# Optimization experiments

Hardware: AMD Instinct MI355X
Metric: run time of the kernel (lower is better)

Reference implementation:

```python
import jax, jax.numpy as jnp
import numpy as np

B, P, Q, O, H = 2048, 32, 65, 16, 32

def setup_inputs() -> dict:
    key = jax.random.key(0)
    ks = jax.random.split(key, 13)
    s1 = 1.0           # fan_in = 1 for Linear(1,H)
    sH = 1.0 / np.sqrt(H)
    return {
        "x": jax.random.normal(ks[0], (B, P), dtype=jnp.float32),
        # psi_{p,q}: 1 -> H -> H -> 1 MLPs, stacked over (P, Q)
        "psi_w1": jax.random.normal(ks[1], (P, Q, H), dtype=jnp.float32) * s1,
        "psi_b1": jax.random.normal(ks[2], (P, Q, H), dtype=jnp.float32) * s1,
        "psi_w2": jax.random.normal(ks[3], (P, Q, H, H), dtype=jnp.float32) * sH,
        "psi_b2": jax.random.normal(ks[4], (P, Q, H), dtype=jnp.float32) * sH,
        "psi_w3": jax.random.normal(ks[5], (P, Q, H), dtype=jnp.float32) * sH,
        "psi_b3": jax.random.normal(ks[6], (P, Q), dtype=jnp.float32) * sH,
        # phi_{q,i}: 1 -> H -> H -> 1 MLPs, stacked over (Q, O)
        "phi_w1": jax.random.normal(ks[7], (Q, O, H), dtype=jnp.float32) * s1,
        "phi_b1": jax.random.normal(ks[8], (Q, O, H), dtype=jnp.float32) * s1,
        "phi_w2": jax.random.normal(ks[9], (Q, O, H, H), dtype=jnp.float32) * sH,
        "phi_b2": jax.random.normal(ks[10], (Q, O, H), dtype=jnp.float32) * sH,
        "phi_w3": jax.random.normal(ks[11], (Q, O, H), dtype=jnp.float32) * sH,
        "phi_b3": jax.random.normal(ks[12], (Q, O), dtype=jnp.float32) * sH,
    }

def reference(x, psi_w1, psi_b1, psi_w2, psi_b2, psi_w3, psi_b3,
              phi_w1, phi_b1, phi_w2, phi_b2, phi_w3, phi_b3):
    # Inner functions psi_{p,q}(x_p): all P*Q tiny MLPs batched together.
    h = jnp.tanh(x[:, :, None, None] * psi_w1 + psi_b1)                 # [B,P,Q,H]
    h = jnp.tanh(jnp.einsum('bpqh,pqhk->bpqk', h, psi_w2) + psi_b2)     # [B,P,Q,H]
    psi = jnp.einsum('bpqh,pqh->bpq', h, psi_w3) + psi_b3               # [B,P,Q]
    s = psi.sum(axis=1)                                                 # [B,Q]  (sum over p)
    # Outer functions phi_{q,i}(s_q): all Q*O tiny MLPs batched together.
    g = jnp.tanh(s[:, :, None, None] * phi_w1 + phi_b1)                 # [B,Q,O,H]
    g = jnp.tanh(jnp.einsum('bqoh,qohk->bqok', g, phi_w2) + phi_b2)     # [B,Q,O,H]
    phi = jnp.einsum('bqoh,qoh->bqo', g, phi_w3) + phi_b3               # [B,Q,O]
    return phi.sum(axis=1)                                              # [B,O]  (sum over q)
```

## Files before the change

kernel.cpp:

```cpp
#include <hip/hip_runtime.h>

#define B_ 2048
#define P_ 32
#define Q_ 65
#define O_ 16
#define H_ 32

typedef __attribute__((ext_vector_type(8))) short short8;
typedef __attribute__((ext_vector_type(4))) float f32x4;

union F4S8 { float4 f; short8 s; };

#if defined(__has_builtin)
# if __has_builtin(__builtin_amdgcn_exp2f)
#  define HAVE_EXP2 1
# endif
#endif
#ifdef HAVE_EXP2
#define SCALE_K 2.8853900817779268f
__device__ __forceinline__ float exp_z(float y) { return __builtin_amdgcn_exp2f(y); }
#else
#define SCALE_K 2.0f
__device__ __forceinline__ float exp_z(float y) { return __expf(y); }
#endif

__device__ __forceinline__ float tanh_pre(float y) {
    float e = exp_z(y);
    return fmaf(-2.0f, __builtin_amdgcn_rcpf(e + 1.0f), 1.0f);
}

__device__ __forceinline__ unsigned short bf_rne(float f) {
    unsigned u = __float_as_uint(f);
    return (unsigned short)((u + 0x7FFFu + ((u >> 16) & 1u)) >> 16);
}

struct Rec {
    float4 w1a, w1b, b1a, b1b;
    float4 h0, l0, h1, l1;
    float4 ms;
};

template<int MODE>
__device__ __forceinline__ Rec load_rec(
    const float* __restrict__ fragc, const float* __restrict__ shw,
    const float* __restrict__ w1, const float* __restrict__ b1,
    const float* __restrict__ w2, const float* __restrict__ b2,
    const float* __restrict__ w3,
    int pq, int lane, int g, int col)
{
    Rec r;
    if (MODE == 2) {
        const float4* fp = reinterpret_cast<const float4*>(fragc) + (size_t)pq * 256 + lane;
        r.h0 = fp[0]; r.l0 = fp[64]; r.h1 = fp[128]; r.l1 = fp[192];
        const float4* a = reinterpret_cast<const float4*>(shw + (size_t)pq * 128);
        r.w1a = a[g * 2];     r.w1b = a[g * 2 + 1];
        r.b1a = a[8 + g * 2]; r.b1b = a[8 + g * 2 + 1];
        r.ms  = a[16 + col];
    } else {
        const float4* w1p = reinterpret_cast<const float4*>(w1 + pq * H_ + g * 8);
        r.w1a = w1p[0]; r.w1b = w1p[1];
        const float4* b1p = reinterpret_cast<const float4*>(b1 + pq * H_ + g * 8);
        r.b1a = b1p[0]; r.b1b = b1p[1];
        const float* w2p = w2 + (size_t)pq * (H_ * H_);
        F4S8 u0, u1, u2, u3;
        #pragma unroll
        for (int jj = 0; jj < 8; ++jj) {
            float v0 = SCALE_K * w2p[(g * 8 + jj) * H_ + col];
            float v1 = SCALE_K * w2p[(g * 8 + jj) * H_ + 16 + col];
            unsigned q0 = __float_as_uint(v0);
            u0.s[jj] = (short)(q0 >> 16);
            u1.s[jj] = (short)(__float_as_uint(v0 - __uint_as_float(q0 & 0xFFFF0000u)) >> 16);
            unsigned q1 = __float_as_uint(v1);
            u2.s[jj] = (short)(q1 >> 16);
            u3.s[jj] = (short)(__float_as_uint(v1 - __uint_as_float(q1 & 0xFFFF0000u)) >> 16);
        }
        r.h0 = u0.f; r.l0 = u1.f; r.h1 = u2.f; r.l1 = u3.f;
        r.ms = make_float4(SCALE_K * b2[pq * H_ + col], SCALE_K * b2[pq * H_ + 16 + col],
                           w3[pq * H_ + col], w3[pq * H_ + 16 + col]);
    }
    return r;
}

template<bool L1_PRESCALED>
__device__ __forceinline__ void eval_rec(const Rec& r, float xv, float psum[4])
{
    short8 ahi, alo;
#define L1STEP(j, W, Bc)                                                    \
    { float zz = fmaf(xv, (W), (Bc));                                       \
      float y  = L1_PRESCALED ? zz : zz * SCALE_K;                          \
      float tt = tanh_pre(y);                                               \
      unsigned uu = __float_as_uint(tt);                                    \
      ahi[j] = (short)(uu >> 16);                                           \
      float ll = tt - __uint_as_float(uu & 0xFFFF0000u);                    \
      alo[j] = (short)(__float_as_uint(ll) >> 16); }
    L1STEP(0, r.w1a.x, r.b1a.x)
    L1STEP(1, r.w1a.y, r.b1a.y)
    L1STEP(2, r.w1a.z, r.b1a.z)
    L1STEP(3, r.w1a.w, r.b1a.w)
    L1STEP(4, r.w1b.x, r.b1b.x)
    L1STEP(5, r.w1b.y, r.b1b.y)
    L1STEP(6, r.w1b.z, r.b1b.z)
    L1STEP(7, r.w1b.w, r.b1b.w)
#undef L1STEP

    F4S8 c0, c1, c2, c3;
    c0.f = r.h0; c1.f = r.l0; c2.f = r.h1; c3.f = r.l1;
    f32x4 acc0 = {r.ms.x, r.ms.x, r.ms.x, r.ms.x};
    f32x4 acc1 = {r.ms.y, r.ms.y, r.ms.y, r.ms.y};
    acc0 = __builtin_amdgcn_mfma_f32_16x16x32_bf16(ahi, c0.s, acc0, 0, 0, 0);
    acc0 = __builtin_amdgcn_mfma_f32_16x16x32_bf16(alo, c0.s, acc0, 0, 0, 0);
    acc0 = __builtin_amdgcn_mfma_f32_16x16x32_bf16(ahi, c1.s, acc0, 0, 0, 0);
    acc1 = __builtin_amdgcn_mfma_f32_16x16x32_bf16(ahi, c2.s, acc1, 0, 0, 0);
    acc1 = __builtin_amdgcn_mfma_f32_16x16x32_bf16(alo, c2.s, acc1, 0, 0, 0);
    acc1 = __builtin_amdgcn_mfma_f32_16x16x32_bf16(ahi, c3.s, acc1, 0, 0, 0);

    #pragma unroll
    for (int rr = 0; rr < 4; ++rr) {
        psum[rr] = fmaf(tanh_pre(acc0[rr]), r.ms.z, psum[rr]);
        psum[rr] = fmaf(tanh_pre(acc1[rr]), r.ms.w, psum[rr]);
    }
}

__device__ __forceinline__ void reduce_store(float psum[4], float b3sum,
                                             int lane, int g, int b0w,
                                             float* addr_base, int stride, bool atomic)
{
    #pragma unroll
    for (int rr = 0; rr < 4; ++rr) {
        psum[rr] += __shfl_xor(psum[rr], 1);
        psum[rr] += __shfl_xor(psum[rr], 2);
        psum[rr] += __shfl_xor(psum[rr], 4);
        psum[rr] += __shfl_xor(psum[rr], 8);
    }
    float v01 = (lane & 1) ? psum[1] : psum[0];
    float v23 = (lane & 1) ? psum[3] : psum[2];
    float v = (lane & 2) ? v23 : v01;
    if ((lane & 15) < 4) {
        int row = b0w + g * 4 + (lane & 3);
        float* a = addr_base + (size_t)row * stride;
        if (atomic) atomicAdd(a, v + b3sum);
        else        *a = v + b3sum;
    }
}

template<int MODE>
__global__ __launch_bounds__(256)
void psi_main(const float* __restrict__ x, const float* __restrict__ xT,
              const float* __restrict__ w1, const float* __restrict__ b1,
              const float* __restrict__ w2, const float* __restrict__ b2,
              const float* __restrict__ w3, const float* __restrict__ b3,
              const float* __restrict__ fragc, const float* __restrict__ shw,
              float* __restrict__ sT)
{
    const int id = blockIdx.x;
    const int j = (id & 7) * 260 + (id >> 3);
    const int q = j >> 5;
    const int btile = j & 31;
    const int lane = threadIdx.x & 63;
    const int wid = threadIdx.x >> 6;
    const int g = lane >> 4, col = lane & 15;
    const int b0w = btile * 64 + wid * 16;

    float psum[4] = {0.f, 0.f, 0.f, 0.f};
    float b3sum = 0.f;

    Rec cur = load_rec<MODE>(fragc, shw, w1, b1, w2, b2, w3, q, lane, g, col);
    float xv = (MODE == 2) ? xT[b0w + col] : x[(size_t)(b0w + col) * P_];

    #pragma unroll 2
    for (int p = 0; p < P_; ++p) {
        const int pn = (p + 1 < P_) ? p + 1 : P_ - 1;
        Rec nxt = load_rec<MODE>(fragc, shw, w1, b1, w2, b2, w3,
                                 pn * Q_ + q, lane, g, col);
        float xn = (MODE == 2) ? xT[(size_t)pn * B_ + b0w + col]
                               : x[(size_t)(b0w + col) * P_ + pn];
        b3sum += b3[p * Q_ + q];
        eval_rec<(MODE == 2)>(cur, xv, psum);
        cur = nxt; xv = xn;
    }

    reduce_store(psum, b3sum, lane, g, b0w, sT + (size_t)q * B_, 1, false);
}

template<int MODE>
__global__ __launch_bounds__(256)
void phi_main(const float* __restrict__ sT,
              const float* __restrict__ w1, const float* __restrict__ b1,
              const float* __restrict__ w2, const float* __restrict__ b2,
              const float* __restrict__ w3, const float* __restrict__ b3,
              const float* __restrict__ fragc, const float* __restrict__ shw,
              float* __restrict__ out)
{
    const int id = blockIdx.x;
    const int j = (id & 7) * 832 + (id >> 3);
    const int qg = j >> 9;
    const int rem = j & 511;
    const int o = rem >> 5;
    const int btile = rem & 31;
    const int lane = threadIdx.x & 63;
    const int wid = threadIdx.x >> 6;
    const int g = lane >> 4, col = lane & 15;
    const int b0w = btile * 64 + wid * 16;

    float psum[4] = {0.f, 0.f, 0.f, 0.f};
    float b3sum = 0.f;

    const int q0 = qg * 5;
    Rec cur = load_rec<MODE>(fragc, shw, w1, b1, w2, b2, w3, q0 * O_ + o, lane, g, col);
    float sv = sT[(size_t)q0 * B_ + b0w + col];

    #pragma unroll
    for (int i = 0; i < 5; ++i) {
        const int in_ = (i + 1 < 5) ? i + 1 : 4;
        const int qn = q0 + in_;
        Rec nxt = load_rec<MODE>(fragc, shw, w1, b1, w2, b2, w3,
                                 qn * O_ + o, lane, g, col);
        float sn = sT[(size_t)qn * B_ + b0w + col];
        b3sum += b3[(q0 + i) * O_ + o];
        eval_rec<(MODE == 2)>(cur, sv, psum);
        cur = nxt; sv = sn;
    }

    reduce_store(psum, b3sum, lane, g, b0w, out + o, O_, true);
}

__global__ __launch_bounds__(256)
void prep_frag(const float* __restrict__ w2, float* __restrict__ frag, int npairs)
{
    int idx = blockIdx.x * 256 + threadIdx.x;
    if (idx >= npairs * 64) return;
    int pq = idx >> 6, lane = idx & 63;
    int g = lane >> 4, col = lane & 15;
    const float* Wp = w2 + (size_t)pq * (H_ * H_);

    short8 h0v, l0v, h1v, l1v;
    #pragma unroll
    for (int jj = 0; jj < 8; ++jj) {
        float v0 = SCALE_K * Wp[(g * 8 + jj) * H_ + col];
        float v1 = SCALE_K * Wp[(g * 8 + jj) * H_ + 16 + col];
        unsigned short hb0 = bf_rne(v0);
        h0v[jj] = (short)hb0;
        l0v[jj] = (short)bf_rne(v0 - __uint_as_float(((unsigned)hb0) << 16));
        unsigned short hb1 = bf_rne(v1);
        h1v[jj] = (short)hb1;
        l1v[jj] = (short)bf_rne(v1 - __uint_as_float(((unsigned)hb1) << 16));
    }
    F4S8 a, b, c, d; a.s = h0v; b.s = l0v; c.s = h1v; d.s = l1v;
    float4* op = reinterpret_cast<float4*>(frag) + (size_t)pq * 256 + lane;
    op[0] = a.f; op[64] = b.f; op[128] = c.f; op[192] = d.f;
}

__global__ __launch_bounds__(256)
void prep_shw(const float* __restrict__ w1, const float* __restrict__ b1,
              const float* __restrict__ b2, const float* __restrict__ w3,
              float* __restrict__ shw, int npairs)
{
    int idx = blockIdx.x * 256 + threadIdx.x;
    if (idx >= npairs * 128) return;
    int pq = idx >> 7, i = idx & 127;
    float v;
    if (i < 32)       v = SCALE_K * w1[pq * H_ + i];
    else if (i < 64)  v = SCALE_K * b1[pq * H_ + (i - 32)];
    else {
        int c = (i - 64) >> 2, rr = i & 3;
        v = (rr == 0) ? SCALE_K * b2[pq * H_ + c]
          : (rr == 1) ? SCALE_K * b2[pq * H_ + c + 16]
          : (rr == 2) ? w3[pq * H_ + c]
          :             w3[pq * H_ + c + 16];
    }
    shw[(size_t)pq * 128 + i] = v;
}

__global__ __launch_bounds__(256)
void prep_xT(const float* __restrict__ x, float* __restrict__ xT)
{
    int idx = blockIdx.x * 256 + threadIdx.x;
    int b = idx >> 5, p = idx & 31;
    xT[(size_t)p * B_ + b] = x[idx];
}

extern "C" void kernel_launch(void* const* d_in, const int* in_sizes, int n_in,
                              void* d_out, int out_size, void* d_ws, size_t ws_size,
                              hipStream_t stream) {
    const float* x      = (const float*)d_in[0];
    const float* psi_w1 = (const float*)d_in[1];
    const float* psi_b1 = (const float*)d_in[2];
    const float* psi_w2 = (const float*)d_in[3];
    const float* psi_b2 = (const float*)d_in[4];
    const float* psi_w3 = (const float*)d_in[5];
    const float* psi_b3 = (const float*)d_in[6];
    const float* phi_w1 = (const float*)d_in[7];
    const float* phi_b1 = (const float*)d_in[8];
    const float* phi_w2 = (const float*)d_in[9];
    const float* phi_b2 = (const float*)d_in[10];
    const float* phi_w3 = (const float*)d_in[11];
    const float* phi_b3 = (const float*)d_in[12];
    float* out = (float*)d_out;

    const size_t ST  = (size_t)B_ * Q_ * sizeof(float);
    const size_t XT  = (size_t)B_ * P_ * sizeof(float);
    const size_t FR1 = (size_t)P_ * Q_ * 64 * 64;
    const size_t FR2 = (size_t)Q_ * O_ * 64 * 64;
    const size_t SH1 = (size_t)P_ * Q_ * 128 * 4;
    const size_t SH2 = (size_t)Q_ * O_ * 128 * 4;

    float* sT = (float*)d_ws;
    hipMemsetAsync(out, 0, (size_t)B_ * O_ * sizeof(float), stream);

    if (ws_size >= ST + XT + FR1 + FR2 + SH1 + SH2) {
        char* base = (char*)d_ws + ST;
        float* xT   = (float*)base;                   base += XT;
        float* fr1  = (float*)base;                   base += FR1;
        float* fr2  = (float*)base;                   base += FR2;
        float* sh1  = (float*)base;                   base += SH1;
        float* sh2  = (float*)base;

        prep_xT<<<(B_ * P_) / 256, 256, 0, stream>>>(x, xT);
        prep_frag<<<(P_ * Q_ * 64 + 255) / 256, 256, 0, stream>>>(psi_w2, fr1, P_ * Q_);
        prep_frag<<<(Q_ * O_ * 64 + 255) / 256, 256, 0, stream>>>(phi_w2, fr2, Q_ * O_);
        prep_shw<<<(P_ * Q_ * 128 + 255) / 256, 256, 0, stream>>>(
            psi_w1, psi_b1, psi_b2, psi_w3, sh1, P_ * Q_);
        prep_shw<<<(Q_ * O_ * 128 + 255) / 256, 256, 0, stream>>>(
            phi_w1, phi_b1, phi_b2, phi_w3, sh2, Q_ * O_);

        psi_main<2><<<2080, 256, 0, stream>>>(
            x, xT, psi_w1, psi_b1, psi_w2, psi_b2, psi_w3, psi_b3, fr1, sh1, sT);
        phi_main<2><<<6656, 256, 0, stream>>>(
            sT, phi_w1, phi_b1, phi_w2, phi_b2, phi_w3, phi_b3, fr2, sh2, out);
    } else {
        psi_main<0><<<2080, 256, 0, stream>>>(
            x, x, psi_w1, psi_b1, psi_w2, psi_b2, psi_w3, psi_b3, sT, sT, sT);
        phi_main<0><<<6656, 256, 0, stream>>>(
            sT, phi_w1, phi_b1, phi_w2, phi_b2, phi_w3, phi_b3, sT, sT, out);
    }
}
```

Before: 226.7 us.

## Fuse prep kernels into one launch, precompute bias sums, regroup phi q-chunks

Merges the five preprocessing kernels into a single prep_all launch that also precomputes summed psi_b3 and phi_b3 biases, so the main loops no longer load b3 every iteration. Phi blocks now process 13 q values each instead of 5, cutting the grid from 6656 to 2560 blocks and cutting atomicAdd contention on the output. This trades fewer launches and atomics for less parallelism in the phi stage and a longer serial loop per block.

```diff
diff --git a/kernel.cpp b/kernel.cpp
--- a/kernel.cpp
+++ b/kernel.cpp
@@ -149,6 +149,7 @@
               const float* __restrict__ w1, const float* __restrict__ b1,
               const float* __restrict__ w2, const float* __restrict__ b2,
               const float* __restrict__ w3, const float* __restrict__ b3,
+              const float* __restrict__ b3c,
               const float* __restrict__ fragc, const float* __restrict__ shw,
               float* __restrict__ sT)
 {
@@ -162,7 +163,7 @@
     const int b0w = btile * 64 + wid * 16;
 
     float psum[4] = {0.f, 0.f, 0.f, 0.f};
-    float b3sum = 0.f;
+    float b3sum = (MODE == 2) ? b3c[q] : 0.f;
 
     Rec cur = load_rec<MODE>(fragc, shw, w1, b1, w2, b2, w3, q, lane, g, col);
     float xv = (MODE == 2) ? xT[b0w + col] : x[(size_t)(b0w + col) * P_];
@@ -174,7 +175,7 @@
                                  pn * Q_ + q, lane, g, col);
         float xn = (MODE == 2) ? xT[(size_t)pn * B_ + b0w + col]
                                : x[(size_t)(b0w + col) * P_ + pn];
-        b3sum += b3[p * Q_ + q];
+        if (MODE != 2) b3sum += b3[p * Q_ + q];
         eval_rec<(MODE == 2)>(cur, xv, psum);
         cur = nxt; xv = xn;
     }
@@ -188,11 +189,12 @@
               const float* __restrict__ w1, const float* __restrict__ b1,
               const float* __restrict__ w2, const float* __restrict__ b2,
               const float* __restrict__ w3, const float* __restrict__ b3,
+              const float* __restrict__ b3g,
               const float* __restrict__ fragc, const float* __restrict__ shw,
               float* __restrict__ out)
 {
     const int id = blockIdx.x;
-    const int j = (id & 7) * 832 + (id >> 3);
+    const int j = (id & 7) * 320 + (id >> 3);
     const int qg = j >> 9;
     const int rem = j & 511;
     const int o = rem >> 5;
@@ -203,20 +205,20 @@
     const int b0w = btile * 64 + wid * 16;
 
     float psum[4] = {0.f, 0.f, 0.f, 0.f};
-    float b3sum = 0.f;
-
-    const int q0 = qg * 5;
+    float b3sum = (MODE == 2) ? b3g[qg * O_ + o] : 0.f;
+
+    const int q0 = qg * 13;
     Rec cur = load_rec<MODE>(fragc, shw, w1, b1, w2, b2, w3, q0 * O_ + o, lane, g, col);
     float sv = sT[(size_t)q0 * B_ + b0w + col];
 
-    #pragma unroll
-    for (int i = 0; i < 5; ++i) {
-        const int in_ = (i + 1 < 5) ? i + 1 : 4;
+    #pragma unroll 2
+    for (int i = 0; i < 13; ++i) {
+        const int in_ = (i + 1 < 13) ? i + 1 : 12;
         const int qn = q0 + in_;
         Rec nxt = load_rec<MODE>(fragc, shw, w1, b1, w2, b2, w3,
                                  qn * O_ + o, lane, g, col);
         float sn = sT[(size_t)qn * B_ + b0w + col];
-        b3sum += b3[(q0 + i) * O_ + o];
+        if (MODE != 2) b3sum += b3[(q0 + i) * O_ + o];
         eval_rec<(MODE == 2)>(cur, sv, psum);
         cur = nxt; sv = sn;
     }
@@ -224,15 +226,12 @@
     reduce_store(psum, b3sum, lane, g, b0w, out + o, O_, true);
 }
 
-__global__ __launch_bounds__(256)
-void prep_frag(const float* __restrict__ w2, float* __restrict__ frag, int npairs)
-{
-    int idx = blockIdx.x * 256 + threadIdx.x;
-    if (idx >= npairs * 64) return;
+__device__ __forceinline__ void do_frag(const float* __restrict__ w2,
+                                        float* __restrict__ frag, int idx)
+{
     int pq = idx >> 6, lane = idx & 63;
     int g = lane >> 4, col = lane & 15;
     const float* Wp = w2 + (size_t)pq * (H_ * H_);
-
     short8 h0v, l0v, h1v, l1v;
     #pragma unroll
     for (int jj = 0; jj < 8; ++jj) {
@@ -250,13 +249,12 @@
     op[0] = a.f; op[64] = b.f; op[128] = c.f; op[192] = d.f;
 }
 
-__global__ __launch_bounds__(256)
-void prep_shw(const float* __restrict__ w1, const float* __restrict__ b1,
-              const float* __restrict__ b2, const float* __restrict__ w3,
-              float* __restrict__ shw, int npairs)
-{
-    int idx = blockIdx.x * 256 + threadIdx.x;
-    if (idx >= npairs * 128) return;
+__device__ __forceinline__ void do_shw(const float* __restrict__ w1,
+                                       const float* __restrict__ b1,
+                                       const float* __restrict__ b2,
+                                       const float* __restrict__ w3,
+                                       float* __restrict__ shw, int idx)
+{
     int pq = idx >> 7, i = idx & 127;
     float v;
     if (i < 32)       v = SCALE_K * w1[pq * H_ + i];
@@ -271,12 +269,57 @@
     shw[(size_t)pq * 128 + i] = v;
 }
 
+#define N1 133120
+#define N2 66560
+#define N3 266240
+#define N4 133120
+#define N5 65536
+#define C1 133120
+#define C2 199680
+#define C3 465920
+#define C4 599040
+#define C5 664576
+#define C6 664641
+#define C7 664721
+
 __global__ __launch_bounds__(256)
-void prep_xT(const float* __restrict__ x, float* __restrict__ xT)
-{
-    int idx = blockIdx.x * 256 + threadIdx.x;
-    int b = idx >> 5, p = idx & 31;
-    xT[(size_t)p * B_ + b] = x[idx];
+void prep_all(const float* __restrict__ psi_w1, const float* __restrict__ psi_b1,
+              const float* __restrict__ psi_w2, const float* __restrict__ psi_b2,
+              const float* __restrict__ psi_w3, const float* __restrict__ psi_b3,
+              const float* __restrict__ phi_w1, const float* __restrict__ phi_b1,
+              const float* __restrict__ phi_w2, const float* __restrict__ phi_b2,
+              const float* __restrict__ phi_w3, const float* __restrict__ phi_b3,
+              const float* __restrict__ x,
+              float* __restrict__ fr1, float* __restrict__ fr2,
+              float* __restrict__ sh1, float* __restrict__ sh2,
+              float* __restrict__ xT, float* __restrict__ b3c,
+              float* __restrict__ b3g)
+{
+    int t = blockIdx.x * 256 + threadIdx.x;
+    if (t < C1) {
+        do_frag(psi_w2, fr1, t);
+    } else if (t < C2) {
+        do_frag(phi_w2, fr2, t - C1);
+    } else if (t < C3) {
+        do_shw(psi_w1, psi_b1, psi_b2, psi_w3, sh1, t - C2);
+    } else if (t < C4) {
+        do_shw(phi_w1, phi_b1, phi_b2, phi_w3, sh2, t - C3);
+    } else if (t < C5) {
+        int idx = t - C4;
+        int b = idx >> 5, p = idx & 31;
+        xT[(size_t)p * B_ + b] = x[idx];
+    } else if (t < C6) {
+        int q = t - C5;
+        float s = 0.f;
+        for (int p = 0; p < P_; ++p) s += psi_b3[p * Q_ + q];
+        b3c[q] = s;
+    } else if (t < C7) {
+        int idx = t - C6;
+        int qg = idx >> 4, o = idx & 15;
+        float s = 0.f;
+        for (int i = 0; i < 13; ++i) s += phi_b3[(qg * 13 + i) * O_ + o];
+        b3g[idx] = s;
+    }
 }
 
 extern "C" void kernel_launch(void* const* d_in, const int* in_sizes, int n_in,
@@ -299,38 +342,43 @@
 
     const size_t ST  = (size_t)B_ * Q_ * sizeof(float);
     const size_t XT  = (size_t)B_ * P_ * sizeof(float);
-    const size_t FR1 = (size_t)P_ * Q_ * 64 * 64;
-    const size_t FR2 = (size_t)Q_ * O_ * 64 * 64;
-    const size_t SH1 = (size_t)P_ * Q_ * 128 * 4;
-    const size_t SH2 = (size_t)Q_ * O_ * 128 * 4;
+    const size_t FR1 = (size_t)N1 * 64;
+    const size_t FR2 = (size_t)N2 * 64;
+    const size_t SH1 = (size_t)N3 * 4;
+    const size_t SH2 = (size_t)N4 * 4;
+    const size_t B3C = 320;
+    const size_t B3G = 320;
 
     float* sT = (float*)d_ws;
     hipMemsetAsync(out, 0, (size_t)B_ * O_ * sizeof(float), stream);
 
-    if (ws_size >= ST + XT + FR1 + FR2 + SH1 + SH2) {
+    if (ws_size >= ST + XT + FR1 + FR2 + SH1 + SH2 + B3C + B3G) {
         char* base = (char*)d_ws + ST;
-        float* xT   = (float*)base;                   base += XT;
+        float* xTp  = (float*)base;                   base += XT;
         float* fr1  = (float*)base;                   base += FR1;
         float* fr2  = (float*)base;                   base += FR2;
         float* sh1  = (float*)base;                   base += SH1;
-        float* sh2  = (float*)base;
-
-        prep_xT<<<(B_ * P_) / 256, 256, 0, stream>>>(x, xT);
-        prep_frag<<<(P_ * Q_ * 64 + 255) / 256, 256, 0, stream>>>(psi_w2, fr1, P_ * Q_);
-        prep_frag<<<(Q_ * O_ * 64 + 255) / 256, 256, 0, stream>>>(phi_w2, fr2, Q_ * O_);
-        prep_shw<<<(P_ * Q_ * 128 + 255) / 256, 256, 0, stream>>>(
-            psi_w1, psi_b1, psi_b2, psi_w3, sh1, P_ * Q_);
-        prep_shw<<<(Q_ * O_ * 128 + 255) / 256, 256, 0, stream>>>(
-            phi_w1, phi_b1, phi_b2, phi_w3, sh2, Q_ * O_);
+        float* sh2  = (float*)base;                   base += SH2;
+        float* b3c  = (float*)base;                   base += B3C;
+        float* b3g  = (float*)base;
+
+        prep_all<<<(C7 + 255) / 256, 256, 0, stream>>>(
+            psi_w1, psi_b1, psi_w2, psi_b2, psi_w3, psi_b3,
+            phi_w1, phi_b1, phi_w2, phi_b2, phi_w3, phi_b3,
+            x, fr1, fr2, sh1, sh2, xTp, b3c, b3g);
 
         psi_main<2><<<2080, 256, 0, stream>>>(
-            x, xT, psi_w1, psi_b1, psi_w2, psi_b2, psi_w3, psi_b3, fr1, sh1, sT);
-        phi_main<2><<<6656, 256, 0, stream>>>(
-            sT, phi_w1, phi_b1, phi_w2, phi_b2, phi_w3, phi_b3, fr2, sh2, out);
+            x, xTp, psi_w1, psi_b1, psi_w2, psi_b2, psi_w3, psi_b3, b3c,
+            fr1, sh1, sT);
+        phi_main<2><<<2560, 256, 0, stream>>>(
+            sT, phi_w1, phi_b1, phi_w2, phi_b2, phi_w3, phi_b3, b3g,
+            fr2, sh2, out);
     } else {
         psi_main<0><<<2080, 256, 0, stream>>>(
-            x, x, psi_w1, psi_b1, psi_w2, psi_b2, psi_w3, psi_b3, sT, sT, sT);
-        phi_main<0><<<6656, 256, 0, stream>>>(
-            sT, phi_w1, phi_b1, phi_w2, phi_b2, phi_w3, phi_b3, sT, sT, out);
-    }
-}
+            x, x, psi_w1, psi_b1, psi_w2, psi_b2, psi_w3, psi_b3, (const float*)sT,
+            sT, sT, sT);
+        phi_main<0><<<2560, 256, 0, stream>>>(
+            sT, phi_w1, phi_b1, phi_w2, phi_b2, phi_w3, phi_b3, (const float*)sT,
+            sT, sT, out);
+    }
+}
```

Measured after the change: 220.3 us. 2.9% less time.
